# Kernel tuning notes

Hardware: AMD Instinct MI355X
Metric: run time of the kernel (lower is better)

The kernel has to match this reference:

```python
import jax, jax.numpy as jnp
import numpy as np

N_IN = 27          # N + 1 (alphabet + blank)
HIDDEN = 1024


def _gru(x, W_ih, W_hh, b_ih, b_hh):
    # x: [B, T, I]; weights follow PyTorch GRU layout (3H rows: r, z, n)
    gi = jnp.einsum('bti,gi->btg', x, W_ih) + b_ih  # [B, T, 3H], input GEMM hoisted out of scan

    def step(h, gi_t):
        gh = h @ W_hh.T + b_hh                      # [B, 3H]
        i_r, i_z, i_n = jnp.split(gi_t, 3, axis=-1)
        h_r, h_z, h_n = jnp.split(gh, 3, axis=-1)
        r = jax.nn.sigmoid(i_r + h_r)
        z = jax.nn.sigmoid(i_z + h_z)
        n = jnp.tanh(i_n + r * h_n)
        h_new = (1.0 - z) * n + z * h
        return h_new, h_new

    h0 = jnp.zeros((x.shape[0], W_hh.shape[1]), x.dtype)
    _, ys = jax.lax.scan(step, h0, jnp.swapaxes(gi, 0, 1))  # scan over time
    return jnp.swapaxes(ys, 0, 1)                            # [B, T, H]


def setup_inputs() -> dict:
    key = jax.random.key(0)
    ks = jax.random.split(key, 8)
    B, T = 64, 1024
    s = 1.0 / np.sqrt(HIDDEN)
    return {
        'x': jax.random.normal(ks[0], (B, T, N_IN), dtype=jnp.float32),
        'delays': jax.random.randint(ks[1], (B,), 0, 16, dtype=jnp.int64),
        'W_ih': jax.random.uniform(ks[2], (3 * HIDDEN, N_IN), jnp.float32, -s, s),
        'W_hh': jax.random.uniform(ks[3], (3 * HIDDEN, HIDDEN), jnp.float32, -s, s),
        'b_ih': jax.random.uniform(ks[4], (3 * HIDDEN,), jnp.float32, -s, s),
        'b_hh': jax.random.uniform(ks[5], (3 * HIDDEN,), jnp.float32, -s, s),
        'W_dec': jax.random.uniform(ks[6], (N_IN, HIDDEN), jnp.float32, -s, s),
        'b_dec': jax.random.uniform(ks[7], (N_IN,), jnp.float32, -s, s),
    }


def reference(x, delays, W_ih, W_hh, b_ih, b_hh, W_dec, b_dec):
    y_hat = _gru(x, W_ih, W_hh, b_ih, b_hh)          # [B, T, H]
    T = x.shape[1]
    j = jnp.arange(T)[None, :]                        # [1, T]
    d = delays[:, None]                               # [B, 1]
    idx = jnp.where(j < d, j, j - d)                  # vectorized delay gather index
    delayed = jnp.take_along_axis(y_hat, idx[:, :, None], axis=1)  # [B, T, H]
    logits = jnp.einsum('bth,oh->bto', delayed, W_dec) + b_dec
    return logits
```

## Files before the change

kernel.cpp:

```cpp
#include <hip/hip_runtime.h>

typedef short bf16x8 __attribute__((ext_vector_type(8)));
typedef float f32x4 __attribute__((ext_vector_type(4)));
typedef unsigned u32x4 __attribute__((ext_vector_type(4)));

#define T_STEPS 1024
#define NBATCH  64
#define HID     1024
#define NIN     27
#define RINGN   32
#define LAG     8
#define BPG     16
#define NWG     256

#define RINGHI_BYTES ((size_t)RINGN * NBATCH * HID * 2)
#define FLAGS_INTS   (NWG * 16)
#define FLAGS_BYTES  ((size_t)FLAGS_INTS * sizeof(int))
#define WS_NEED      (RINGHI_BYTES + FLAGS_BYTES)

__device__ __forceinline__ unsigned short f2bf(float f) {
    unsigned u = __float_as_uint(f);
    unsigned r = u + 0x7FFFu + ((u >> 16) & 1u);
    return (unsigned short)(r >> 16);
}
__device__ __forceinline__ float bf2f(unsigned short h) {
    return __uint_as_float(((unsigned)h) << 16);
}

__device__ __forceinline__ void ld_b128_sys(const void* p, u32x4& v) {
    asm volatile("global_load_dwordx4 %0, %1, off sc0 sc1" : "=v"(v) : "v"(p));
}
__device__ __forceinline__ void ld_b32_sys(const void* p, unsigned& v) {
    asm volatile("global_load_dword %0, %1, off sc0 sc1" : "=v"(v) : "v"(p));
}
__device__ __forceinline__ int ld_flag_sys(const int* p) {
    int v;
    asm volatile("global_load_dword %0, %1, off sc0 sc1\n\ts_waitcnt vmcnt(0)"
                 : "=v"(v) : "v"(p) : "memory");
    return v;
}
__device__ __forceinline__ void st_b32_sys(void* p, unsigned v) {
    asm volatile("global_store_dword %0, %1, off sc0 sc1" :: "v"(p), "v"(v) : "memory");
}
__device__ __forceinline__ void wait_vm0() {
    asm volatile("s_waitcnt vmcnt(0)" ::: "memory");
    __builtin_amdgcn_sched_barrier(0);
}

__global__ __launch_bounds__(256, 1)
void gru_persist(const float* __restrict__ x,
                 const int* __restrict__ delays,
                 const float* __restrict__ W_ih,
                 const float* __restrict__ W_hh,
                 const float* __restrict__ b_ih,
                 const float* __restrict__ b_hh,
                 const float* __restrict__ W_dec,
                 float* __restrict__ out,
                 unsigned short* __restrict__ ring_hi,
                 int* __restrict__ flags)
{
    const int tid  = threadIdx.x;
    const int lane = tid & 63;
    const int kq   = tid >> 6;
    const int gb   = blockIdx.x >> 6;
    const int gs   = blockIdx.x & 63;
    const int j0   = gs * 16;
    const int l15  = lane & 15;
    const int lhi  = lane >> 4;

    __shared__ f32x4 red[13 * 64];
    __shared__ float ylds[2][256];
    __shared__ float bias_lds[64];

    bf16x8 wHH[3][8];
    #pragma unroll
    for (int n = 0; n < 3; ++n) {
        const float* wrow = W_hh + (size_t)(n * HID + j0 + l15) * HID;
        #pragma unroll
        for (int c = 0; c < 8; ++c) {
            const float* wr = wrow + kq * 256 + c * 32 + lhi * 8;
            #pragma unroll
            for (int jj = 0; jj < 8; ++jj) wHH[n][c][jj] = (short)f2bf(wr[jj]);
        }
    }
    bf16x8 wXH[3];
    #pragma unroll
    for (int n = 0; n < 3; ++n) {
        const float* wrow = W_ih + (size_t)(n * HID + j0 + l15) * NIN;
        #pragma unroll
        for (int jj = 0; jj < 8; ++jj) {
            const int kk = lhi * 8 + jj;
            wXH[n][jj] = (kk < NIN) ? (short)f2bf(wrow[kk]) : (short)0;
        }
    }
    if (tid < 16) {
        bias_lds[tid]      = b_ih[j0 + tid] + b_hh[j0 + tid];
        bias_lds[16 + tid] = b_ih[HID + j0 + tid] + b_hh[HID + j0 + tid];
        bias_lds[32 + tid] = b_ih[2 * HID + j0 + tid];
        bias_lds[48 + tid] = b_hh[2 * HID + j0 + tid];
    }
    const int bdec  = gb * BPG + (gs >> 2);
    const int qdec  = gs & 3;
    const int d_del = delays[bdec];
    const int odec  = tid & 31;
    const int jgd   = tid >> 5;
    float wd[32];
    #pragma unroll
    for (int jj = 0; jj < 32; ++jj)
        wd[jj] = (odec < NIN) ? W_dec[(size_t)odec * HID + qdec * 256 + jgd * 32 + jj] : 0.f;

    const int jl = l15;
    const int bl = kq * 4 + lhi;
    const int arow = gb * BPG + l15;

    int* myflag = flags + (gb * 64 + gs) * 16;
    const int* pollflag = flags + (gb * 64 + kq * 16 + l15) * 16;

    float hprev = 0.f;
    bool dead = false;

    __syncthreads();

    #pragma clang loop unroll(disable)
    for (int t = 0; t < T_STEPS + LAG; ++t) {
        const int target = (t < T_STEPS) ? t : T_STEPS;
        const int t_dec  = t - LAG;
        const int slot_prev = (t + RINGN - 1) & (RINGN - 1);

        unsigned ydw = 0;
        if (t_dec >= 0 && tid < 128) {
            const int tau = (t_dec < d_del) ? t_dec : (t_dec - d_del);
            const unsigned* yrow = (const unsigned*)(ring_hi
                + ((size_t)((tau & (RINGN - 1)) * NBATCH + bdec)) * HID + qdec * 256);
            ld_b32_sys(yrow + tid, ydw);
        }
        bf16x8 axH = {}, axL = {};
        if (t < T_STEPS && kq == 0) {
            const float* xr = x + ((size_t)arow * T_STEPS + t) * NIN;
            #pragma unroll
            for (int jj = 0; jj < 8; ++jj) {
                const int kk = lhi * 8 + jj;
                if (kk < NIN) {
                    float f = xr[kk];
                    unsigned short hi = f2bf(f);
                    axH[jj] = (short)hi;
                    axL[jj] = (short)f2bf(f - bf2f(hi));
                }
            }
        }
        __builtin_amdgcn_sched_barrier(0);

        if (target > 0 && !dead) {
            int iter = 0;
            for (;;) {
                int v = target;
                if (lane < 16) v = ld_flag_sys(pollflag);
                if (__all(v >= target)) break;
                if (++iter > (1 << 16)) { dead = true; break; }
            }
        }
        wait_vm0();

        u32x4 rawH[8];
        if (t < T_STEPS) {
            const unsigned short* aH = ring_hi + ((size_t)(slot_prev * NBATCH + arow)) * HID
                                     + kq * 256 + lhi * 8;
            #pragma unroll
            for (int c = 0; c < 8; ++c) ld_b128_sys(aH + c * 32, rawH[c]);
        }

        f32x4 z4 = {0.f, 0.f, 0.f, 0.f};
        f32x4 acc0 = z4, acc1 = z4, acc2 = z4, acc2x = z4;

        if (t < T_STEPS) {
            if (kq == 0) {
                acc0  = __builtin_amdgcn_mfma_f32_16x16x32_bf16(axH, wXH[0], acc0, 0, 0, 0);
                acc1  = __builtin_amdgcn_mfma_f32_16x16x32_bf16(axH, wXH[1], acc1, 0, 0, 0);
                acc2x = __builtin_amdgcn_mfma_f32_16x16x32_bf16(axH, wXH[2], acc2x, 0, 0, 0);
                acc0  = __builtin_amdgcn_mfma_f32_16x16x32_bf16(axL, wXH[0], acc0, 0, 0, 0);
                acc1  = __builtin_amdgcn_mfma_f32_16x16x32_bf16(axL, wXH[1], acc1, 0, 0, 0);
                acc2x = __builtin_amdgcn_mfma_f32_16x16x32_bf16(axL, wXH[2], acc2x, 0, 0, 0);
            }
            wait_vm0();
            #pragma unroll
            for (int c = 0; c < 8; ++c) {
                bf16x8 a = __builtin_bit_cast(bf16x8, rawH[c]);
                acc0 = __builtin_amdgcn_mfma_f32_16x16x32_bf16(a, wHH[0][c], acc0, 0, 0, 0);
                acc1 = __builtin_amdgcn_mfma_f32_16x16x32_bf16(a, wHH[1][c], acc1, 0, 0, 0);
                acc2 = __builtin_amdgcn_mfma_f32_16x16x32_bf16(a, wHH[2][c], acc2, 0, 0, 0);
            }
            red[(0 * 4 + kq) * 64 + lane] = acc0;
            red[(1 * 4 + kq) * 64 + lane] = acc1;
            red[(2 * 4 + kq) * 64 + lane] = acc2;
            if (kq == 0) red[12 * 64 + lane] = acc2x;
        } else {
            wait_vm0();
        }
        if (t_dec >= 0 && tid < 128) {
            ylds[t & 1][2 * tid]     = bf2f((unsigned short)(ydw & 0xFFFFu));
            ylds[t & 1][2 * tid + 1] = bf2f((unsigned short)(ydw >> 16));
        }
        __syncthreads();

        if (t < T_STEPS) {
            const float* redf = (const float*)red;
            const int ridx = (jl + 16 * (bl >> 2)) * 4 + (bl & 3);
            float gr = 0.f, gz = 0.f, gh_n = 0.f;
            #pragma unroll
            for (int w = 0; w < 4; ++w) {
                gr   += redf[((0 * 4 + w) * 64) * 4 + ridx];
                gz   += redf[((1 * 4 + w) * 64) * 4 + ridx];
                gh_n += redf[((2 * 4 + w) * 64) * 4 + ridx];
            }
            const float i_n = redf[(12 * 64) * 4 + ridx];
            const float r  = 1.f / (1.f + __expf(-(gr + bias_lds[jl])));
            const float z  = 1.f / (1.f + __expf(-(gz + bias_lds[16 + jl])));
            const float nn = tanhf(i_n + bias_lds[32 + jl] + r * (gh_n + bias_lds[48 + jl]));
            const float hnew = (1.f - z) * nn + z * hprev;
            hprev = hnew;
            const unsigned short hih = f2bf(hnew);
            const unsigned nhi = __shfl_xor((unsigned)hih, 1);
            if ((l15 & 1) == 0) {
                const unsigned dhi = (unsigned)hih | (nhi << 16);
                const int bg = gb * BPG + bl;
                unsigned short* ph = ring_hi
                    + ((size_t)((t & (RINGN - 1)) * NBATCH + bg)) * HID + j0 + jl;
                st_b32_sys(ph, dhi);
            }
        }
        float pdec = 0.f;
        if (t_dec >= 0) {
            if (odec < NIN) {
                const float* yrow = ylds[t & 1] + jgd * 32;
                #pragma unroll
                for (int k = 0; k < 32; ++k) pdec += yrow[k] * wd[k];
            }
            pdec += __shfl_xor(pdec, 32);
        }
        wait_vm0();
        __syncthreads();

        if (t < T_STEPS && tid == 0 && !dead)
            st_b32_sys(myflag, (unsigned)(t + 1));

        if (t_dec >= 0 && lane < 32 && odec < NIN)
            atomicAdd(out + ((size_t)bdec * T_STEPS + t_dec) * NIN + odec, pdec);
    }
}

__global__ void fill_out_kernel(float* __restrict__ out, const float* __restrict__ b_dec, int n)
{
    int idx = blockIdx.x * blockDim.x + threadIdx.x;
    if (idx < n) out[idx] = b_dec[idx % NIN];
}

extern "C" void kernel_launch(void* const* d_in, const int* in_sizes, int n_in,
                              void* d_out, int out_size, void* d_ws, size_t ws_size,
                              hipStream_t stream)
{
    (void)in_sizes; (void)n_in;
    const float* xx    = (const float*)d_in[0];
    const int*   dl    = (const int*)d_in[1];
    const float* W_ih  = (const float*)d_in[2];
    const float* W_hh  = (const float*)d_in[3];
    const float* b_ih  = (const float*)d_in[4];
    const float* b_hh  = (const float*)d_in[5];
    const float* W_dec = (const float*)d_in[6];
    const float* b_dec = (const float*)d_in[7];
    float* out = (float*)d_out;

    if (ws_size < WS_NEED) return;

    unsigned short* ring_hi = (unsigned short*)d_ws;
    int*            flags   = (int*)((char*)d_ws + RINGHI_BYTES);

    const size_t slot_bytes = (size_t)NBATCH * HID * 2;
    hipMemsetAsync((char*)d_ws + (size_t)(RINGN - 1) * slot_bytes, 0,
                   slot_bytes + FLAGS_BYTES, stream);

    fill_out_kernel<<<dim3((out_size + 255) / 256), dim3(256), 0, stream>>>(out, b_dec, out_size);

    void* args[] = {(void*)&xx, (void*)&dl, (void*)&W_ih, (void*)&W_hh, (void*)&b_ih,
                    (void*)&b_hh, (void*)&W_dec, (void*)&out, (void*)&ring_hi, (void*)&flags};
    hipError_t e = hipLaunchCooperativeKernel((void*)gru_persist, dim3(NWG), dim3(256),
                                              args, 0, stream);
    if (e != hipSuccess) {
        gru_persist<<<dim3(NWG), dim3(256), 0, stream>>>(xx, dl, W_ih, W_hh, b_ih, b_hh,
                                                         W_dec, out, ring_hi, flags);
    }
}
```

Baseline: 3.965 ms.

## Replace per-step flag barrier with sentinel-tagged ring data polling

Drops the separate per-workgroup progress flags and the second __syncthreads per step. Consumers now poll the hidden-state ring slot itself for a NaN sentinel value, and each producer re-poisons the slot seven steps ahead. The reduction LDS buffer is double-buffered so the trailing barrier can go, and the input MFMAs are issued before polling. This cuts one barrier and one flag store/load round trip from the serial critical path. The cost is a full ring-initialisation kernel, validation of every loaded dword, and a correctness risk if a real bf16 pair ever equals the sentinel or if slot reuse races.

```diff
diff --git a/kernel.cpp b/kernel.cpp
--- a/kernel.cpp
+++ b/kernel.cpp
@@ -12,11 +12,11 @@
 #define LAG     8
 #define BPG     16
 #define NWG     256
-
-#define RINGHI_BYTES ((size_t)RINGN * NBATCH * HID * 2)
-#define FLAGS_INTS   (NWG * 16)
-#define FLAGS_BYTES  ((size_t)FLAGS_INTS * sizeof(int))
-#define WS_NEED      (RINGHI_BYTES + FLAGS_BYTES)
+#define SENT    0x7FC07FC0u
+
+#define RING_DWORDS ((size_t)RINGN * NBATCH * HID / 2)
+#define SLOT_DWORDS ((size_t)NBATCH * HID / 2)
+#define WS_NEED     (RING_DWORDS * 4)
 
 __device__ __forceinline__ unsigned short f2bf(float f) {
     unsigned u = __float_as_uint(f);
@@ -33,8 +33,8 @@
 __device__ __forceinline__ void ld_b32_sys(const void* p, unsigned& v) {
     asm volatile("global_load_dword %0, %1, off sc0 sc1" : "=v"(v) : "v"(p));
 }
-__device__ __forceinline__ int ld_flag_sys(const int* p) {
-    int v;
+__device__ __forceinline__ unsigned ld_poll_sys(const unsigned* p) {
+    unsigned v;
     asm volatile("global_load_dword %0, %1, off sc0 sc1\n\ts_waitcnt vmcnt(0)"
                  : "=v"(v) : "v"(p) : "memory");
     return v;
@@ -56,8 +56,7 @@
                  const float* __restrict__ b_hh,
                  const float* __restrict__ W_dec,
                  float* __restrict__ out,
-                 unsigned short* __restrict__ ring_hi,
-                 int* __restrict__ flags)
+                 unsigned short* __restrict__ ring_hi)
 {
     const int tid  = threadIdx.x;
     const int lane = tid & 63;
@@ -67,8 +66,9 @@
     const int j0   = gs * 16;
     const int l15  = lane & 15;
     const int lhi  = lane >> 4;
-
-    __shared__ f32x4 red[13 * 64];
+    const int Bg   = gb * BPG;
+
+    __shared__ f32x4 red[2][13 * 64];
     __shared__ float ylds[2][256];
     __shared__ float bias_lds[64];
 
@@ -111,10 +111,8 @@
 
     const int jl = l15;
     const int bl = kq * 4 + lhi;
-    const int arow = gb * BPG + l15;
-
-    int* myflag = flags + (gb * 64 + gs) * 16;
-    const int* pollflag = flags + (gb * 64 + kq * 16 + l15) * 16;
+    const int arow = Bg + l15;
+    const unsigned* ringdw = (const unsigned*)ring_hi;
 
     float hprev = 0.f;
     bool dead = false;
@@ -123,20 +121,21 @@
 
     #pragma clang loop unroll(disable)
     for (int t = 0; t < T_STEPS + LAG; ++t) {
-        const int target = (t < T_STEPS) ? t : T_STEPS;
         const int t_dec  = t - LAG;
         const int slot_prev = (t + RINGN - 1) & (RINGN - 1);
 
         unsigned ydw = 0;
         if (t_dec >= 0 && tid < 128) {
             const int tau = (t_dec < d_del) ? t_dec : (t_dec - d_del);
-            const unsigned* yrow = (const unsigned*)(ring_hi
-                + ((size_t)((tau & (RINGN - 1)) * NBATCH + bdec)) * HID + qdec * 256);
+            const unsigned* yrow = ringdw
+                + ((size_t)((tau & (RINGN - 1)) * NBATCH + bdec)) * (HID / 2) + qdec * 128;
             ld_b32_sys(yrow + tid, ydw);
         }
-        bf16x8 axH = {}, axL = {};
+        f32x4 z4 = {0.f, 0.f, 0.f, 0.f};
+        f32x4 acc0 = z4, acc1 = z4, acc2 = z4, acc2x = z4;
         if (t < T_STEPS && kq == 0) {
             const float* xr = x + ((size_t)arow * T_STEPS + t) * NIN;
+            bf16x8 axH = {}, axL = {};
             #pragma unroll
             for (int jj = 0; jj < 8; ++jj) {
                 const int kk = lhi * 8 + jj;
@@ -147,16 +146,25 @@
                     axL[jj] = (short)f2bf(f - bf2f(hi));
                 }
             }
+            acc0  = __builtin_amdgcn_mfma_f32_16x16x32_bf16(axH, wXH[0], acc0, 0, 0, 0);
+            acc1  = __builtin_amdgcn_mfma_f32_16x16x32_bf16(axH, wXH[1], acc1, 0, 0, 0);
+            acc2x = __builtin_amdgcn_mfma_f32_16x16x32_bf16(axH, wXH[2], acc2x, 0, 0, 0);
+            acc0  = __builtin_amdgcn_mfma_f32_16x16x32_bf16(axL, wXH[0], acc0, 0, 0, 0);
+            acc1  = __builtin_amdgcn_mfma_f32_16x16x32_bf16(axL, wXH[1], acc1, 0, 0, 0);
+            acc2x = __builtin_amdgcn_mfma_f32_16x16x32_bf16(axL, wXH[2], acc2x, 0, 0, 0);
         }
         __builtin_amdgcn_sched_barrier(0);
 
-        if (target > 0 && !dead) {
+        if (t < T_STEPS && !dead) {
+            const unsigned* pollp = ringdw
+                + ((size_t)(slot_prev * NBATCH + Bg + l15)) * (HID / 2)
+                + kq * 128 + l15 * 8;
             int iter = 0;
             for (;;) {
-                int v = target;
-                if (lane < 16) v = ld_flag_sys(pollflag);
-                if (__all(v >= target)) break;
-                if (++iter > (1 << 16)) { dead = true; break; }
+                unsigned v = 0;
+                if (lane < 16) v = ld_poll_sys(pollp);
+                if (__all(v != SENT)) break;
+                if (++iter > (1 << 17)) { dead = true; break; }
             }
         }
         wait_vm0();
@@ -165,23 +173,19 @@
         if (t < T_STEPS) {
             const unsigned short* aH = ring_hi + ((size_t)(slot_prev * NBATCH + arow)) * HID
                                      + kq * 256 + lhi * 8;
-            #pragma unroll
-            for (int c = 0; c < 8; ++c) ld_b128_sys(aH + c * 32, rawH[c]);
-        }
-
-        f32x4 z4 = {0.f, 0.f, 0.f, 0.f};
-        f32x4 acc0 = z4, acc1 = z4, acc2 = z4, acc2x = z4;
-
-        if (t < T_STEPS) {
-            if (kq == 0) {
-                acc0  = __builtin_amdgcn_mfma_f32_16x16x32_bf16(axH, wXH[0], acc0, 0, 0, 0);
-                acc1  = __builtin_amdgcn_mfma_f32_16x16x32_bf16(axH, wXH[1], acc1, 0, 0, 0);
-                acc2x = __builtin_amdgcn_mfma_f32_16x16x32_bf16(axH, wXH[2], acc2x, 0, 0, 0);
-                acc0  = __builtin_amdgcn_mfma_f32_16x16x32_bf16(axL, wXH[0], acc0, 0, 0, 0);
-                acc1  = __builtin_amdgcn_mfma_f32_16x16x32_bf16(axL, wXH[1], acc1, 0, 0, 0);
-                acc2x = __builtin_amdgcn_mfma_f32_16x16x32_bf16(axL, wXH[2], acc2x, 0, 0, 0);
-            }
-            wait_vm0();
+            int vr = 0;
+            for (;;) {
+                #pragma unroll
+                for (int c = 0; c < 8; ++c) ld_b128_sys(aH + c * 32, rawH[c]);
+                wait_vm0();
+                bool ok = true;
+                #pragma unroll
+                for (int c = 0; c < 8; ++c)
+                    #pragma unroll
+                    for (int d = 0; d < 4; ++d) ok &= (rawH[c][d] != SENT);
+                if (__all(ok)) break;
+                if (++vr > 1024) { dead = true; break; }
+            }
             #pragma unroll
             for (int c = 0; c < 8; ++c) {
                 bf16x8 a = __builtin_bit_cast(bf16x8, rawH[c]);
@@ -189,12 +193,10 @@
                 acc1 = __builtin_amdgcn_mfma_f32_16x16x32_bf16(a, wHH[1][c], acc1, 0, 0, 0);
                 acc2 = __builtin_amdgcn_mfma_f32_16x16x32_bf16(a, wHH[2][c], acc2, 0, 0, 0);
             }
-            red[(0 * 4 + kq) * 64 + lane] = acc0;
-            red[(1 * 4 + kq) * 64 + lane] = acc1;
-            red[(2 * 4 + kq) * 64 + lane] = acc2;
-            if (kq == 0) red[12 * 64 + lane] = acc2x;
-        } else {
-            wait_vm0();
+            red[t & 1][(0 * 4 + kq) * 64 + lane] = acc0;
+            red[t & 1][(1 * 4 + kq) * 64 + lane] = acc1;
+            red[t & 1][(2 * 4 + kq) * 64 + lane] = acc2;
+            if (kq == 0) red[t & 1][12 * 64 + lane] = acc2x;
         }
         if (t_dec >= 0 && tid < 128) {
             ylds[t & 1][2 * tid]     = bf2f((unsigned short)(ydw & 0xFFFFu));
@@ -203,7 +205,7 @@
         __syncthreads();
 
         if (t < T_STEPS) {
-            const float* redf = (const float*)red;
+            const float* redf = (const float*)&red[t & 1][0];
             const int ridx = (jl + 16 * (bl >> 2)) * 4 + (bl & 3);
             float gr = 0.f, gz = 0.f, gh_n = 0.f;
             #pragma unroll
@@ -222,30 +224,33 @@
             const unsigned nhi = __shfl_xor((unsigned)hih, 1);
             if ((l15 & 1) == 0) {
                 const unsigned dhi = (unsigned)hih | (nhi << 16);
-                const int bg = gb * BPG + bl;
-                unsigned short* ph = ring_hi
-                    + ((size_t)((t & (RINGN - 1)) * NBATCH + bg)) * HID + j0 + jl;
+                const int bg = Bg + bl;
+                const size_t dwoff = (size_t)bg * (HID / 2) + ((j0 + jl) >> 1);
+                unsigned* ph = (unsigned*)ring_hi + (size_t)(t & (RINGN - 1)) * SLOT_DWORDS + dwoff;
+                unsigned* pp = (unsigned*)ring_hi + (size_t)((t + 7) & (RINGN - 1)) * SLOT_DWORDS + dwoff;
                 st_b32_sys(ph, dhi);
-            }
-        }
-        float pdec = 0.f;
+                st_b32_sys(pp, SENT);
+            }
+        }
         if (t_dec >= 0) {
+            float pdec = 0.f;
             if (odec < NIN) {
                 const float* yrow = ylds[t & 1] + jgd * 32;
                 #pragma unroll
                 for (int k = 0; k < 32; ++k) pdec += yrow[k] * wd[k];
             }
             pdec += __shfl_xor(pdec, 32);
-        }
-        wait_vm0();
-        __syncthreads();
-
-        if (t < T_STEPS && tid == 0 && !dead)
-            st_b32_sys(myflag, (unsigned)(t + 1));
-
-        if (t_dec >= 0 && lane < 32 && odec < NIN)
-            atomicAdd(out + ((size_t)bdec * T_STEPS + t_dec) * NIN + odec, pdec);
-    }
+            if (lane < 32 && odec < NIN)
+                atomicAdd(out + ((size_t)bdec * T_STEPS + t_dec) * NIN + odec, pdec);
+        }
+    }
+}
+
+__global__ void fill_ring_kernel(unsigned* __restrict__ ring)
+{
+    const size_t i = (size_t)blockIdx.x * blockDim.x + threadIdx.x;
+    if (i < RING_DWORDS)
+        ring[i] = (i >= (RINGN - 1) * SLOT_DWORDS) ? 0u : SENT;
 }
 
 __global__ void fill_out_kernel(float* __restrict__ out, const float* __restrict__ b_dec, int n)
@@ -272,20 +277,17 @@
     if (ws_size < WS_NEED) return;
 
     unsigned short* ring_hi = (unsigned short*)d_ws;
-    int*            flags   = (int*)((char*)d_ws + RINGHI_BYTES);
-
-    const size_t slot_bytes = (size_t)NBATCH * HID * 2;
-    hipMemsetAsync((char*)d_ws + (size_t)(RINGN - 1) * slot_bytes, 0,
-                   slot_bytes + FLAGS_BYTES, stream);
-
+
+    fill_ring_kernel<<<dim3((unsigned)((RING_DWORDS + 255) / 256)), dim3(256), 0, stream>>>(
+        (unsigned*)d_ws);
     fill_out_kernel<<<dim3((out_size + 255) / 256), dim3(256), 0, stream>>>(out, b_dec, out_size);
 
     void* args[] = {(void*)&xx, (void*)&dl, (void*)&W_ih, (void*)&W_hh, (void*)&b_ih,
-                    (void*)&b_hh, (void*)&W_dec, (void*)&out, (void*)&ring_hi, (void*)&flags};
+                    (void*)&b_hh, (void*)&W_dec, (void*)&out, (void*)&ring_hi};
     hipError_t e = hipLaunchCooperativeKernel((void*)gru_persist, dim3(NWG), dim3(256),
                                               args, 0, stream);
     if (e != hipSuccess) {
         gru_persist<<<dim3(NWG), dim3(256), 0, stream>>>(xx, dl, W_ih, W_hh, b_ih, b_hh,
-                                                         W_dec, out, ring_hi, flags);
-    }
-}
+                                                         W_dec, out, ring_hi);
+    }
+}
```

After: 4.016 ms. No clear change (+1.3%).

## Halve persistent workgroup count with 512-thread groups covering 32 hidden columns

Applied to the files above, without the earlier changes.

Repartitions the persistent GRU from 256 workgroups of 256 threads to 128 workgroups of 512 threads. Each workgroup now owns 32 hidden columns split into two 16-column MFMA tiles, with the K dimension split across 8 waves instead of 4. This halves the number of flags each group polls per step (4 lanes instead of 16). The decoder partials are reduced in shared memory before a single atomicAdd per output, so fewer atomics are issued. The cost is a larger cross-wave LDS reduction and a 512-thread barrier every timestep.

```diff
diff --git a/kernel.cpp b/kernel.cpp
--- a/kernel.cpp
+++ b/kernel.cpp
@@ -11,7 +11,8 @@
 #define RINGN   32
 #define LAG     8
 #define BPG     16
-#define NWG     256
+#define NWG     128
+#define WGSZ    512
 
 #define RINGHI_BYTES ((size_t)RINGN * NBATCH * HID * 2)
 #define FLAGS_INTS   (NWG * 16)
@@ -47,7 +48,7 @@
     __builtin_amdgcn_sched_barrier(0);
 }
 
-__global__ __launch_bounds__(256, 1)
+__global__ __launch_bounds__(WGSZ, 1)
 void gru_persist(const float* __restrict__ x,
                  const int* __restrict__ delays,
                  const float* __restrict__ W_ih,
@@ -62,59 +63,67 @@
     const int tid  = threadIdx.x;
     const int lane = tid & 63;
     const int kq   = tid >> 6;
-    const int gb   = blockIdx.x >> 6;
-    const int gs   = blockIdx.x & 63;
-    const int j0   = gs * 16;
+    const int gb   = blockIdx.x >> 5;
+    const int gs   = blockIdx.x & 31;
+    const int j0   = gs * 32;
     const int l15  = lane & 15;
     const int lhi  = lane >> 4;
-
-    __shared__ f32x4 red[13 * 64];
-    __shared__ float ylds[2][256];
-    __shared__ float bias_lds[64];
-
-    bf16x8 wHH[3][8];
+    const int Bg   = gb * BPG;
+
+    __shared__ f32x4 red[48 * 64];
+    __shared__ f32x4 inx[2 * 64];
+    __shared__ float ylds[2][512];
+    __shared__ float decp[256];
+    __shared__ float bias_lds[128];
+
+    bf16x8 wHH[3][2][4];
     #pragma unroll
-    for (int n = 0; n < 3; ++n) {
-        const float* wrow = W_hh + (size_t)(n * HID + j0 + l15) * HID;
+    for (int n = 0; n < 3; ++n)
         #pragma unroll
-        for (int c = 0; c < 8; ++c) {
-            const float* wr = wrow + kq * 256 + c * 32 + lhi * 8;
-            #pragma unroll
-            for (int jj = 0; jj < 8; ++jj) wHH[n][c][jj] = (short)f2bf(wr[jj]);
-        }
+        for (int ct = 0; ct < 2; ++ct) {
+            const float* wrow = W_hh + (size_t)(n * HID + j0 + ct * 16 + l15) * HID;
+            #pragma unroll
+            for (int c = 0; c < 4; ++c) {
+                const float* wr = wrow + kq * 128 + c * 32 + lhi * 8;
+                #pragma unroll
+                for (int jj = 0; jj < 8; ++jj) wHH[n][ct][c][jj] = (short)f2bf(wr[jj]);
+            }
+        }
+    bf16x8 wXH[3][2];
+    #pragma unroll
+    for (int n = 0; n < 3; ++n)
+        #pragma unroll
+        for (int ct = 0; ct < 2; ++ct) {
+            const float* wrow = W_ih + (size_t)(n * HID + j0 + ct * 16 + l15) * NIN;
+            #pragma unroll
+            for (int jj = 0; jj < 8; ++jj) {
+                const int kk = lhi * 8 + jj;
+                wXH[n][ct][jj] = (kk < NIN) ? (short)f2bf(wrow[kk]) : (short)0;
+            }
+        }
+    if (tid < 32) {
+        bias_lds[tid]      = b_ih[j0 + tid] + b_hh[j0 + tid];
+        bias_lds[32 + tid] = b_ih[HID + j0 + tid] + b_hh[HID + j0 + tid];
+        bias_lds[64 + tid] = b_ih[2 * HID + j0 + tid];
+        bias_lds[96 + tid] = b_hh[2 * HID + j0 + tid];
     }
-    bf16x8 wXH[3];
-    #pragma unroll
-    for (int n = 0; n < 3; ++n) {
-        const float* wrow = W_ih + (size_t)(n * HID + j0 + l15) * NIN;
-        #pragma unroll
-        for (int jj = 0; jj < 8; ++jj) {
-            const int kk = lhi * 8 + jj;
-            wXH[n][jj] = (kk < NIN) ? (short)f2bf(wrow[kk]) : (short)0;
-        }
-    }
-    if (tid < 16) {
-        bias_lds[tid]      = b_ih[j0 + tid] + b_hh[j0 + tid];
-        bias_lds[16 + tid] = b_ih[HID + j0 + tid] + b_hh[HID + j0 + tid];
-        bias_lds[32 + tid] = b_ih[2 * HID + j0 + tid];
-        bias_lds[48 + tid] = b_hh[2 * HID + j0 + tid];
-    }
-    const int bdec  = gb * BPG + (gs >> 2);
-    const int qdec  = gs & 3;
+    const int bdec  = Bg + (gs >> 1);
+    const int qdec  = gs & 1;
     const int d_del = delays[bdec];
     const int odec  = tid & 31;
     const int jgd   = tid >> 5;
     float wd[32];
     #pragma unroll
     for (int jj = 0; jj < 32; ++jj)
-        wd[jj] = (odec < NIN) ? W_dec[(size_t)odec * HID + qdec * 256 + jgd * 32 + jj] : 0.f;
-
-    const int jl = l15;
-    const int bl = kq * 4 + lhi;
-    const int arow = gb * BPG + l15;
-
-    int* myflag = flags + (gb * 64 + gs) * 16;
-    const int* pollflag = flags + (gb * 64 + kq * 16 + l15) * 16;
+        wd[jj] = (odec < NIN) ? W_dec[(size_t)odec * HID + qdec * 512 + jgd * 32 + jj] : 0.f;
+
+    const int bl = tid >> 5;
+    const int jc = tid & 31;
+    const int arow = Bg + l15;
+    const unsigned* ringdw = (const unsigned*)ring_hi;
+
+    int* myflag = flags + blockIdx.x * 16;
+    const int* pollflag = flags + (gb * 32 + kq * 4 + (lane & 3)) * 16;
 
     float hprev = 0.f;
     bool dead = false;
@@ -128,10 +137,10 @@
         const int slot_prev = (t + RINGN - 1) & (RINGN - 1);
 
         unsigned ydw = 0;
-        if (t_dec >= 0 && tid < 128) {
+        if (t_dec >= 0 && tid < 256) {
             const int tau = (t_dec < d_del) ? t_dec : (t_dec - d_del);
-            const unsigned* yrow = (const unsigned*)(ring_hi
-                + ((size_t)((tau & (RINGN - 1)) * NBATCH + bdec)) * HID + qdec * 256);
+            const unsigned* yrow = ringdw
+                + ((size_t)((tau & (RINGN - 1)) * NBATCH + bdec)) * (HID / 2) + qdec * 256;
             ld_b32_sys(yrow + tid, ydw);
         }
         bf16x8 axH = {}, axL = {};
@@ -154,88 +163,104 @@
             int iter = 0;
             for (;;) {
                 int v = target;
-                if (lane < 16) v = ld_flag_sys(pollflag);
+                if (lane < 4) v = ld_flag_sys(pollflag);
                 if (__all(v >= target)) break;
                 if (++iter > (1 << 16)) { dead = true; break; }
             }
         }
         wait_vm0();
 
-        u32x4 rawH[8];
+        u32x4 rawH[4];
         if (t < T_STEPS) {
             const unsigned short* aH = ring_hi + ((size_t)(slot_prev * NBATCH + arow)) * HID
-                                     + kq * 256 + lhi * 8;
-            #pragma unroll
-            for (int c = 0; c < 8; ++c) ld_b128_sys(aH + c * 32, rawH[c]);
+                                     + kq * 128 + lhi * 8;
+            #pragma unroll
+            for (int c = 0; c < 4; ++c) ld_b128_sys(aH + c * 32, rawH[c]);
         }
 
         f32x4 z4 = {0.f, 0.f, 0.f, 0.f};
-        f32x4 acc0 = z4, acc1 = z4, acc2 = z4, acc2x = z4;
+        f32x4 acc[3][2] = {{z4, z4}, {z4, z4}, {z4, z4}};
+        f32x4 accx[2] = {z4, z4};
 
         if (t < T_STEPS) {
             if (kq == 0) {
-                acc0  = __builtin_amdgcn_mfma_f32_16x16x32_bf16(axH, wXH[0], acc0, 0, 0, 0);
-                acc1  = __builtin_amdgcn_mfma_f32_16x16x32_bf16(axH, wXH[1], acc1, 0, 0, 0);
-                acc2x = __builtin_amdgcn_mfma_f32_16x16x32_bf16(axH, wXH[2], acc2x, 0, 0, 0);
-                acc0  = __builtin_amdgcn_mfma_f32_16x16x32_bf16(axL, wXH[0], acc0, 0, 0, 0);
-                acc1  = __builtin_amdgcn_mfma_f32_16x16x32_bf16(axL, wXH[1], acc1, 0, 0, 0);
-                acc2x = __builtin_amdgcn_mfma_f32_16x16x32_bf16(axL, wXH[2], acc2x, 0, 0, 0);
+                #pragma unroll
+                for (int ct = 0; ct < 2; ++ct) {
+                    acc[0][ct] = __builtin_amdgcn_mfma_f32_16x16x32_bf16(axH, wXH[0][ct], acc[0][ct], 0, 0, 0);
+                    acc[1][ct] = __builtin_amdgcn_mfma_f32_16x16x32_bf16(axH, wXH[1][ct], acc[1][ct], 0, 0, 0);
+                    accx[ct]   = __builtin_amdgcn_mfma_f32_16x16x32_bf16(axH, wXH[2][ct], accx[ct], 0, 0, 0);
+                    acc[0][ct] = __builtin_amdgcn_mfma_f32_16x16x32_bf16(axL, wXH[0][ct], acc[0][ct], 0, 0, 0);
+                    acc[1][ct] = __builtin_amdgcn_mfma_f32_16x16x32_bf16(axL, wXH[1][ct], acc[1][ct], 0, 0, 0);
+                    accx[ct]   = __builtin_amdgcn_mfma_f32_16x16x32_bf16(axL, wXH[2][ct], accx[ct], 0, 0, 0);
+                }
             }
             wait_vm0();
             #pragma unroll
-            for (int c = 0; c < 8; ++c) {
+            for (int c = 0; c < 4; ++c) {
                 bf16x8 a = __builtin_bit_cast(bf16x8, rawH[c]);
-                acc0 = __builtin_amdgcn_mfma_f32_16x16x32_bf16(a, wHH[0][c], acc0, 0, 0, 0);
-                acc1 = __builtin_amdgcn_mfma_f32_16x16x32_bf16(a, wHH[1][c], acc1, 0, 0, 0);
-                acc2 = __builtin_amdgcn_mfma_f32_16x16x32_bf16(a, wHH[2][c], acc2, 0, 0, 0);
-            }
-            red[(0 * 4 + kq) * 64 + lane] = acc0;
-            red[(1 * 4 + kq) * 64 + lane] = acc1;
-            red[(2 * 4 + kq) * 64 + lane] = acc2;
-            if (kq == 0) red[12 * 64 + lane] = acc2x;
+                #pragma unroll
+                for (int ct = 0; ct < 2; ++ct) {
+                    acc[0][ct] = __builtin_amdgcn_mfma_f32_16x16x32_bf16(a, wHH[0][ct][c], acc[0][ct], 0, 0, 0);
+                    acc[1][ct] = __builtin_amdgcn_mfma_f32_16x16x32_bf16(a, wHH[1][ct][c], acc[1][ct], 0, 0, 0);
+                    acc[2][ct] = __builtin_amdgcn_mfma_f32_16x16x32_bf16(a, wHH[2][ct][c], acc[2][ct], 0, 0, 0);
+                }
+            }
+            #pragma unroll
+            for (int n = 0; n < 3; ++n)
+                #pragma unroll
+                for (int ct = 0; ct < 2; ++ct)
+                    red[((n * 2 + ct) * 8 + kq) * 64 + lane] = acc[n][ct];
+            if (kq == 0) {
+                inx[0 * 64 + lane] = accx[0];
+                inx[1 * 64 + lane] = accx[1];
+            }
         } else {
             wait_vm0();
         }
-        if (t_dec >= 0 && tid < 128) {
+        if (t_dec >= 0 && tid < 256) {
             ylds[t & 1][2 * tid]     = bf2f((unsigned short)(ydw & 0xFFFFu));
             ylds[t & 1][2 * tid + 1] = bf2f((unsigned short)(ydw >> 16));
         }
         __syncthreads();
 
         if (t < T_STEPS) {
+            const int ct   = jc >> 4;
+            const int c16  = jc & 15;
+            const int ridx = (c16 + 16 * (bl >> 2)) * 4 + (bl & 3);
             const float* redf = (const float*)red;
-            const int ridx = (jl + 16 * (bl >> 2)) * 4 + (bl & 3);
             float gr = 0.f, gz = 0.f, gh_n = 0.f;
             #pragma unroll
-            for (int w = 0; w < 4; ++w) {
-                gr   += redf[((0 * 4 + w) * 64) * 4 + ridx];
-                gz   += redf[((1 * 4 + w) * 64) * 4 + ridx];
-                gh_n += redf[((2 * 4 + w) * 64) * 4 + ridx];
-            }
-            const float i_n = redf[(12 * 64) * 4 + ridx];
-            const float r  = 1.f / (1.f + __expf(-(gr + bias_lds[jl])));
-            const float z  = 1.f / (1.f + __expf(-(gz + bias_lds[16 + jl])));
-            const float nn = tanhf(i_n + bias_lds[32 + jl] + r * (gh_n + bias_lds[48 + jl]));
+            for (int w = 0; w < 8; ++w) {
+                gr   += redf[((0 * 2 + ct) * 8 + w) * 256 + ridx];
+                gz   += redf[((1 * 2 + ct) * 8 + w) * 256 + ridx];
+                gh_n += redf[((2 * 2 + ct) * 8 + w) * 256 + ridx];
+            }
+            const float i_n = ((const float*)inx)[ct * 256 + ridx];
+            const float r  = 1.f / (1.f + __expf(-(gr + bias_lds[jc])));
+            const float z  = 1.f / (1.f + __expf(-(gz + bias_lds[32 + jc])));
+            const float nn = tanhf(i_n + bias_lds[64 + jc] + r * (gh_n + bias_lds[96 + jc]));
             const float hnew = (1.f - z) * nn + z * hprev;
             hprev = hnew;
             const unsigned short hih = f2bf(hnew);
             const unsigned nhi = __shfl_xor((unsigned)hih, 1);
-            if ((l15 & 1) == 0) {
+            if ((jc & 1) == 0) {
                 const unsigned dhi = (unsigned)hih | (nhi << 16);
-                const int bg = gb * BPG + bl;
-                unsigned short* ph = ring_hi
-                    + ((size_t)((t & (RINGN - 1)) * NBATCH + bg)) * HID + j0 + jl;
+                const int bg = Bg + bl;
+                unsigned* ph = (unsigned*)ring_hi
+                    + ((size_t)((t & (RINGN - 1)) * NBATCH + bg)) * (HID / 2)
+                    + ((j0 + jc) >> 1);
                 st_b32_sys(ph, dhi);
             }
         }
-        float pdec = 0.f;
         if (t_dec >= 0) {
+            float p = 0.f;
             if (odec < NIN) {
                 const float* yrow = ylds[t & 1] + jgd * 32;
                 #pragma unroll
-                for (int k = 0; k < 32; ++k) pdec += yrow[k] * wd[k];
-            }
-            pdec += __shfl_xor(pdec, 32);
+                for (int k = 0; k < 32; ++k) p += yrow[k] * wd[k];
+            }
+            p += __shfl_xor(p, 32);
+            if (lane < 32) decp[kq * 32 + (lane & 31)] = p;
         }
         wait_vm0();
         __syncthreads();
@@ -243,8 +268,12 @@
         if (t < T_STEPS && tid == 0 && !dead)
             st_b32_sys(myflag, (unsigned)(t + 1));
 
-        if (t_dec >= 0 && lane < 32 && odec < NIN)
-            atomicAdd(out + ((size_t)bdec * T_STEPS + t_dec) * NIN + odec, pdec);
+        if (t_dec >= 0 && tid < NIN) {
+            float v = 0.f;
+            #pragma unroll
+            for (int w = 0; w < 8; ++w) v += decp[w * 32 + tid];
+            atomicAdd(out + ((size_t)bdec * T_STEPS + t_dec) * NIN + tid, v);
+        }
     }
 }
 
@@ -282,10 +311,10 @@
 
     void* args[] = {(void*)&xx, (void*)&dl, (void*)&W_ih, (void*)&W_hh, (void*)&b_ih,
                     (void*)&b_hh, (void*)&W_dec, (void*)&out, (void*)&ring_hi, (void*)&flags};
-    hipError_t e = hipLaunchCooperativeKernel((void*)gru_persist, dim3(NWG), dim3(256),
+    hipError_t e = hipLaunchCooperativeKernel((void*)gru_persist, dim3(NWG), dim3(WGSZ),
                                               args, 0, stream);
     if (e != hipSuccess) {
-        gru_persist<<<dim3(NWG), dim3(256), 0, stream>>>(xx, dl, W_ih, W_hh, b_ih, b_hh,
-                                                         W_dec, out, ring_hi, flags);
+        gru_persist<<<dim3(NWG), dim3(WGSZ), 0, stream>>>(xx, dl, W_ih, W_hh, b_ih, b_hh,
+                                                          W_dec, out, ring_hi, flags);
     }
 }
```

Result: slower. 6.660 ms (+68.0%).
